# Optimization experiments

Measured on AMD Instinct MI355X. Metric: run time of the kernel, lower is better.

Reference implementation:

```python
import jax, jax.numpy as jnp
import numpy as np

N = 50000          # nodes
E = 800000         # edges (avg degree 16)
NODE_IN, NODE_OUT = 64, 96
EDGE_IN, EDGE_OUT = 32, 32
CONV = [192, 192]  # hidden_conv_sizes
LIN = [192]        # hidden_linear_sizes
NUM_CLASSES = 2


def _linear_init(k, fan_in, fan_out):
    s = 1.0 / np.sqrt(fan_in)
    kw, kb = jax.random.split(k)
    W = jax.random.uniform(kw, (fan_in, fan_out), jnp.float32, -s, s)
    b = jax.random.uniform(kb, (fan_out,), jnp.float32, -s, s)
    return W, b


def setup_inputs() -> dict:
    key = jax.random.key(0)
    ks = jax.random.split(key, 10)
    node_feats = jax.random.normal(ks[0], (N, NODE_IN), jnp.float32)
    edge_feats = jax.random.normal(ks[1], (E, EDGE_IN), jnp.float32)
    src = jax.random.randint(ks[2], (E,), 0, N)
    dst = jax.random.randint(ks[3], (E,), 0, N)
    Wn, bn = _linear_init(ks[4], NODE_IN, NODE_OUT)
    We, be = _linear_init(ks[5], EDGE_IN, EDGE_OUT)
    Wc0, bc0 = _linear_init(ks[6], NODE_OUT + EDGE_OUT, CONV[0])
    Wc1, bc1 = _linear_init(ks[7], CONV[0], CONV[1])
    Wl0, bl0 = _linear_init(ks[8], CONV[1], LIN[0])
    Wo, bo = _linear_init(ks[9], LIN[0], NUM_CLASSES)
    return dict(node_feats=node_feats, edge_feats=edge_feats,
                Wn=Wn, bn=bn, We=We, be=be,
                Wc0=Wc0, bc0=bc0, Wc1=Wc1, bc1=bc1,
                Wl0=Wl0, bl0=bl0, Wo=Wo, bo=bo,
                src=src, dst=dst)


def reference(node_feats, edge_feats, Wn, bn, We, be, Wc0, bc0, Wc1, bc1,
              Wl0, bl0, Wo, bo, src, dst):
    ones = jnp.ones((E,), jnp.float32)
    deg_in = jnp.clip(jax.ops.segment_sum(ones, dst, num_segments=N), 1.0)
    deg_out = jnp.clip(jax.ops.segment_sum(ones, src, num_segments=N), 1.0)
    inv_in = jax.lax.rsqrt(deg_in)    # D_in^{-1/2}
    inv_out = jax.lax.rsqrt(deg_out)  # D_out^{-1/2}

    # EdgeLayer: per-edge linear, mean-aggregated onto destination nodes
    eh = edge_feats @ We + be                                   # [E, EDGE_OUT]
    edge_h = jax.nn.relu(
        jax.ops.segment_sum(eh, dst, num_segments=N) / deg_in[:, None])

    # NodeEmbeddingLayer: per-node linear
    node_h = jax.nn.relu(node_feats @ Wn + bn)                  # [N, NODE_OUT]

    h = jnp.concatenate([edge_h, node_h], axis=1)               # [N, EDGE_OUT+NODE_OUT]

    # dgl GraphConv (norm='both'): D_in^{-1/2} A D_out^{-1/2} h W + b
    # dropout is identity in eval mode
    for W, b in ((Wc0, bc0), (Wc1, bc1)):
        msg = (h * inv_out[:, None])[src]                       # [E, d] gather
        agg = jax.ops.segment_sum(msg, dst, num_segments=N) * inv_in[:, None]
        h = jax.nn.relu(agg @ W + b)

    h = jax.nn.relu(h @ Wl0 + bl0)
    return h @ Wo + bo                                          # [N, NUM_CLASSES]
```

## Files before the change

### kernel.cpp

```cpp
#include <hip/hip_runtime.h>

#define NN 50000
#define NE 800000
#define CAP 64

#define NPB 128
#define NBKT 391
#define NBKT_PAD 512
#define BCAP 3072
#define CHUNK 4096

typedef unsigned short u16;
typedef unsigned long long u64;
typedef __attribute__((ext_vector_type(8))) short bf8_t;
typedef __attribute__((ext_vector_type(4))) float f4_t;

__device__ __forceinline__ u16 f2b(float f) {
    unsigned u = __float_as_uint(f);
    unsigned r = u + 0x7FFF + ((u >> 16) & 1);
    return (u16)(r >> 16);
}

__global__ __launch_bounds__(256) void partition_k(
    const int* __restrict__ src, const int* __restrict__ dst,
    int* __restrict__ deg_out, int* __restrict__ bktc,
    u64* __restrict__ part, int E) {
    __shared__ unsigned cnt[NBKT_PAD];
    __shared__ unsigned base[NBKT_PAD];
    __shared__ unsigned cur[NBKT_PAD];
    __shared__ unsigned gbase[NBKT_PAD];
    __shared__ unsigned wtot[4];
    __shared__ u64 staged[CHUNK];

    const int tid = threadIdx.x;
    const int lane = tid & 63;
    const int wid = tid >> 6;
    const int e0 = blockIdx.x * CHUNK;
    const int n = min(CHUNK, E - e0);

    for (int i = tid; i < NBKT_PAD; i += 256) cnt[i] = 0;
    __syncthreads();

    for (int i = tid; i < n; i += 256) {
        int d = dst[e0 + i];
        atomicAdd(&cnt[d >> 7], 1u);
    }
    __syncthreads();

    {
        unsigned a = cnt[2 * tid];
        unsigned b = cnt[2 * tid + 1];
        unsigned ps = a + b;
        unsigned inc = ps;
#pragma unroll
        for (int d = 1; d < 64; d <<= 1) {
            unsigned v = __shfl_up(inc, d);
            if (lane >= d) inc += v;
        }
        if (lane == 63) wtot[wid] = inc;
        __syncthreads();
        unsigned wb = 0;
#pragma unroll
        for (int k = 0; k < 4; ++k) wb += (k < wid) ? wtot[k] : 0;
        unsigned eb = wb + inc - ps;
        base[2 * tid] = eb;
        base[2 * tid + 1] = eb + a;
        cur[2 * tid] = eb;
        cur[2 * tid + 1] = eb + a;
    }
    __syncthreads();

    for (int i = tid; i < n; i += 256) {
        int e = e0 + i;
        int d = dst[e];
        int s = src[e];
        atomicAdd(deg_out + s, 1);
        unsigned p = atomicAdd(&cur[d >> 7], 1u);
        staged[p] = ((u64)(unsigned)e << 32) | (((unsigned)d << 16) | (unsigned)s);
    }
    __syncthreads();

    for (int b = tid; b < NBKT; b += 256) {
        unsigned c = cur[b] - base[b];
        if (c) gbase[b] = (unsigned)atomicAdd(&bktc[b], (int)c);
    }
    __syncthreads();

    for (int i = tid; i < n; i += 256) {
        u64 v = staged[i];
        int b = (int)((v >> 16) & 0xffffu) >> 7;
        unsigned idx = gbase[b] + ((unsigned)i - base[b]);
        if (idx < BCAP) part[(size_t)b * BCAP + idx] = v;
    }
}

__global__ __launch_bounds__(256) void fill_k(
    const u64* __restrict__ part, const int* __restrict__ bktc,
    int2* __restrict__ csr, int* __restrict__ din, int n) {
    __shared__ unsigned cur[NPB];
    const int tid = threadIdx.x;
    const int b = blockIdx.x;
    const int node0 = b << 7;
    if (tid < NPB) cur[tid] = 0;
    __syncthreads();

    const int cnt = min(bktc[b], BCAP);
    const u64* p = part + (size_t)b * BCAP;
    for (int i = tid; i < cnt; i += 256) {
        u64 v = p[i];
        int s = (int)(v & 0xffffu);
        int d = (int)((v >> 16) & 0xffffu);
        int e = (int)(v >> 32);
        unsigned q = atomicAdd(&cur[d & (NPB - 1)], 1u);
        if (q < CAP) csr[((size_t)d << 6) + q] = make_int2(s, e);
    }
    __syncthreads();
    int node = node0 + tid;
    if (tid < NPB && node < n) din[node] = (int)cur[tid];
}

__global__ void make_inv_k(const int* __restrict__ deg_in, const int* __restrict__ deg_out,
                           float* __restrict__ inv_in, float* __restrict__ inv_out,
                           float* __restrict__ inv_mean, float* __restrict__ bcoef, int n) {
    int i = blockIdx.x * 256 + threadIdx.x;
    if (i < n) {
        int d_in = deg_in[i];
        float di = fmaxf((float)d_in, 1.0f);
        float dq = fmaxf((float)deg_out[i], 1.0f);
        inv_in[i]   = 1.0f / sqrtf(di);
        inv_out[i]  = 1.0f / sqrtf(dq);
        inv_mean[i] = 1.0f / di;
        bcoef[i]    = (d_in > 0) ? 1.0f : 0.0f;
    }
}

__global__ __launch_bounds__(256) void gather_e2_k(
    const float* __restrict__ ef, const int2* __restrict__ csr,
    const int* __restrict__ deg, float* __restrict__ efa) {
    const int lane = threadIdx.x & 63;
    const int node = __builtin_amdgcn_readfirstlane(blockIdx.x * 4 + (threadIdx.x >> 6));
    const int beg = node << 6;
    const int cnt = deg[node];
    const int off = lane & 31;
    const int half = lane >> 5;
    float acc = 0.0f;

    const int np = cnt >> 1;
    const int nb = np >> 3, rem = np & 7;
    int idx[8];
    if (nb > 0) {
#pragma unroll
        for (int j = 0; j < 8; ++j) idx[j] = csr[beg + 2 * j + half].y;
    }
    for (int b = 0; b < nb; ++b) {
        float lv[8];
#pragma unroll
        for (int j = 0; j < 8; ++j) lv[j] = ef[(size_t)idx[j] * 32 + off];
        int nidx[8];
        const int nbase = beg + 2 * (b + 1) * 8;
        if (b + 1 < nb) {
#pragma unroll
            for (int j = 0; j < 8; ++j) nidx[j] = csr[nbase + 2 * j + half].y;
        }
#pragma unroll
        for (int j = 0; j < 8; ++j) acc += lv[j];
        if (b + 1 < nb) {
#pragma unroll
            for (int j = 0; j < 8; ++j) idx[j] = nidx[j];
        }
    }
    const int tbase = beg + 2 * nb * 8;
    for (int t = 0; t < rem; ++t) acc += ef[(size_t)csr[tbase + 2 * t + half].y * 32 + off];
    if ((cnt & 1) && half == 0) acc += ef[(size_t)csr[beg + cnt - 1].y * 32 + off];

    acc += __shfl_down(acc, 32);
    if (lane < 32) efa[(size_t)node * 32 + off] = acc;
}

template <int D, int LPT>
__global__ __launch_bounds__(256) void gather_b2_k(
    const u16* __restrict__ h, const int2* __restrict__ csr,
    const int* __restrict__ deg, const float* __restrict__ inv_in,
    u16* __restrict__ agg) {
    constexpr int ACT = D / LPT;
    constexpr int NW = LPT / 2;
    const int lane = threadIdx.x & 63;
    const int node = __builtin_amdgcn_readfirstlane(blockIdx.x * 4 + (threadIdx.x >> 6));
    const int beg = node << 6;
    const int cnt = deg[node];
    const int off = (lane < ACT ? lane : ACT - 1) * LPT;

    float acc[LPT];
#pragma unroll
    for (int j = 0; j < LPT; ++j) acc[j] = 0.0f;

    const int nb = cnt >> 4;
    int idx[16];
    if (nb > 0) {
#pragma unroll
        for (int j = 0; j < 16; ++j) idx[j] = csr[beg + j].x;
    }
    for (int b = 0; b < nb; ++b) {
        unsigned lv[16][NW];
#pragma unroll
        for (int j = 0; j < 16; ++j) {
            const unsigned* p = (const unsigned*)(h + (size_t)idx[j] * D + off);
            if constexpr (NW == 2) {
                uint2 t = *(const uint2*)p;
                lv[j][0] = t.x; lv[j][1] = t.y;
            } else {
                lv[j][0] = *p;
            }
        }
        int nidx[16];
        const int nbase = beg + (b + 1) * 16;
        if (b + 1 < nb) {
#pragma unroll
            for (int j = 0; j < 16; ++j) nidx[j] = csr[nbase + j].x;
        }
#pragma unroll
        for (int j = 0; j < 16; ++j)
#pragma unroll
            for (int q = 0; q < NW; ++q) {
                unsigned u = lv[j][q];
                acc[2 * q]     += __uint_as_float(u << 16);
                acc[2 * q + 1] += __uint_as_float(u & 0xffff0000u);
            }
        if (b + 1 < nb) {
#pragma unroll
            for (int j = 0; j < 16; ++j) idx[j] = nidx[j];
        }
    }

    int tb = beg + (nb << 4);
    int rem = cnt & 15;
    if (rem >= 8) {
        int ti[8];
#pragma unroll
        for (int j = 0; j < 8; ++j) ti[j] = csr[tb + j].x;
        unsigned lv[8][NW];
#pragma unroll
        for (int j = 0; j < 8; ++j) {
            const unsigned* p = (const unsigned*)(h + (size_t)ti[j] * D + off);
            if constexpr (NW == 2) {
                uint2 t = *(const uint2*)p;
                lv[j][0] = t.x; lv[j][1] = t.y;
            } else {
                lv[j][0] = *p;
            }
        }
#pragma unroll
        for (int j = 0; j < 8; ++j)
#pragma unroll
            for (int q = 0; q < NW; ++q) {
                unsigned u = lv[j][q];
                acc[2 * q]     += __uint_as_float(u << 16);
                acc[2 * q + 1] += __uint_as_float(u & 0xffff0000u);
            }
        tb += 8;
        rem -= 8;
    }
    for (int t = 0; t < rem; ++t) {
        const unsigned* p = (const unsigned*)(h + (size_t)csr[tb + t].x * D + off);
#pragma unroll
        for (int q = 0; q < NW; ++q) {
            unsigned u = p[q];
            acc[2 * q]     += __uint_as_float(u << 16);
            acc[2 * q + 1] += __uint_as_float(u & 0xffff0000u);
        }
    }

    if (lane < ACT) {
        float sc = inv_in[node];
        unsigned o[NW];
#pragma unroll
        for (int q = 0; q < NW; ++q)
            o[q] = (unsigned)f2b(acc[2 * q] * sc) | ((unsigned)f2b(acc[2 * q + 1] * sc) << 16);
        unsigned* dp = (unsigned*)(agg + (size_t)node * D + off);
        if constexpr (NW == 2) {
            uint2 t; t.x = o[0]; t.y = o[1];
            *(uint2*)dp = t;
        } else {
            *dp = o[0];
        }
    }
}

template <int D_IN, int D_OUT, bool SCALE, bool BROW>
__global__ __launch_bounds__(256) void gemm_tile_k(
    const float* __restrict__ in, int in_stride,
    const float* __restrict__ W, const float* __restrict__ bias,
    const float* __restrict__ scale, const float* __restrict__ brow,
    const float* __restrict__ posts,
    u16* __restrict__ out, int out_stride, int n) {
    constexpr int TMW = 8;
    constexpr int ROWS = TMW * 4;
    constexpr int NOUT = (D_OUT + 63) / 64;
    __shared__ float s_in[ROWS * D_IN];

    const int tid = threadIdx.x;
    const int lane = tid & 63;
    const int wave = tid >> 6;
    const int row0 = blockIdx.x * ROWS;

    constexpr int NV = ROWS * D_IN / 4;
    for (int i = tid; i < NV; i += 256) {
        int m = i / (D_IN / 4);
        int kv = i % (D_IN / 4);
        int row = min(row0 + m, n - 1);
        float4 v = *(const float4*)(in + (size_t)row * in_stride + kv * 4);
        if (SCALE) {
            float s = scale[row];
            v.x *= s; v.y *= s; v.z *= s; v.w *= s;
        }
        *(float4*)(s_in + m * D_IN + kv * 4) = v;
    }
    __syncthreads();

    int f[NOUT], ff[NOUT];
    bool fok[NOUT];
    float bv[NOUT];
#pragma unroll
    for (int o = 0; o < NOUT; ++o) {
        f[o] = lane + 64 * o;
        fok[o] = (f[o] < D_OUT);
        ff[o] = fok[o] ? f[o] : 0;
        bv[o] = bias[ff[o]];
    }

    const float* s_my = s_in + wave * TMW * D_IN;

    float acc[NOUT][TMW];
#pragma unroll
    for (int o = 0; o < NOUT; ++o)
#pragma unroll
        for (int m = 0; m < TMW; ++m) acc[o][m] = 0.0f;

    for (int k = 0; k < D_IN; k += 4) {
        float w[4][NOUT];
#pragma unroll
        for (int j = 0; j < 4; ++j)
#pragma unroll
            for (int o = 0; o < NOUT; ++o) w[j][o] = W[(k + j) * D_OUT + ff[o]];
#pragma unroll
        for (int m = 0; m < TMW; ++m) {
            float4 a = *(const float4*)(s_my + m * D_IN + k);
#pragma unroll
            for (int o = 0; o < NOUT; ++o) {
                acc[o][m] = fmaf(a.x, w[0][o], acc[o][m]);
                acc[o][m] = fmaf(a.y, w[1][o], acc[o][m]);
                acc[o][m] = fmaf(a.z, w[2][o], acc[o][m]);
                acc[o][m] = fmaf(a.w, w[3][o], acc[o][m]);
            }
        }
    }

#pragma unroll
    for (int m = 0; m < TMW; ++m) {
        int row = row0 + wave * TMW + m;
        if (row < n) {
            float bc = BROW ? brow[row] : 1.0f;
            float pm = posts[row];
#pragma unroll
            for (int o = 0; o < NOUT; ++o) {
                if (!fok[o]) continue;
                float v = fmaxf(acc[o][m] + bv[o] * bc, 0.0f) * pm;
                out[(size_t)row * out_stride + f[o]] = f2b(v);
            }
        }
    }
}

template <int K>
__global__ void pack_w_k(const float* __restrict__ W, u16* __restrict__ Wp) {
    constexpr int KS = K / 32;
    int idx = blockIdx.x * 256 + threadIdx.x;
    if (idx >= 12 * KS * 64) return;
    int l = idx & 63;
    int s = (idx >> 6) % KS;
    int t = (idx >> 6) / KS;
    int col = t * 16 + (l & 15);
    int krow = s * 32 + ((l >> 4) * 8);
    u16 tmp[8] __attribute__((aligned(16)));
#pragma unroll
    for (int j = 0; j < 8; ++j) tmp[j] = f2b(W[(size_t)(krow + j) * 192 + col]);
    *(uint4*)(Wp + (size_t)idx * 8) = *(const uint4*)tmp;
}

template <int K>
__global__ __launch_bounds__(256) void mfma_gemm_k(
    const u16* __restrict__ A, const u16* __restrict__ Wp,
    const float* __restrict__ bias, const float* __restrict__ posts,
    u16* __restrict__ outB, int n) {
    constexpr int KS = K / 32;
    const int tid = threadIdx.x;
    const int lane = tid & 63;
    const int w = tid >> 6;
    const int row0 = blockIdx.x * 16;
    const int arow = row0 + (lane & 15);
    const int kbase = (lane >> 4) * 8;

    f4_t acc[3];
#pragma unroll
    for (int o = 0; o < 3; ++o) acc[o] = (f4_t){0.f, 0.f, 0.f, 0.f};

    const u16* ap = A + (size_t)arow * K + kbase;
#pragma unroll
    for (int s = 0; s < KS; ++s) {
        bf8_t af = *(const bf8_t*)(ap + s * 32);
#pragma unroll
        for (int o = 0; o < 3; ++o) {
            int t = w * 3 + o;
            bf8_t bf = *(const bf8_t*)(Wp + (size_t)((t * KS + s) * 64 + lane) * 8);
            acc[o] = __builtin_amdgcn_mfma_f32_16x16x32_bf16(af, bf, acc[o], 0, 0, 0);
        }
    }

    const int drow = row0 + (lane >> 4) * 4;
    const int dcol = lane & 15;
    float pm[4];
#pragma unroll
    for (int r = 0; r < 4; ++r) pm[r] = posts[drow + r];
#pragma unroll
    for (int o = 0; o < 3; ++o) {
        int col = (w * 3 + o) * 16 + dcol;
        float bv = bias[col];
#pragma unroll
        for (int r = 0; r < 4; ++r) {
            float v = fmaxf(acc[o][r] + bv, 0.0f) * pm[r];
            outB[(size_t)(drow + r) * 192 + col] = f2b(v);
        }
    }
}

__global__ __launch_bounds__(256) void mfma_fused_k(
    const u16* __restrict__ A,
    const u16* __restrict__ Wp1, const float* __restrict__ b1,
    const u16* __restrict__ Wp2, const float* __restrict__ b2,
    const float* __restrict__ Wo, const float* __restrict__ bo,
    float* __restrict__ out, int n) {
    constexpr int KS = 6;
    constexpr int S = 200;
    __shared__ float sbuf[16 * S];
    __shared__ float s_head[16][17][2];

    const int tid = threadIdx.x;
    const int lane = tid & 63;
    const int w = tid >> 6;
    const int row0 = blockIdx.x * 16;
    const int arow = row0 + (lane & 15);
    const int kbase = (lane >> 4) * 8;
    const int drow = (lane >> 4) * 4;
    const int dcol = lane & 15;

    f4_t acc[3];
#pragma unroll
    for (int o = 0; o < 3; ++o) acc[o] = (f4_t){0.f, 0.f, 0.f, 0.f};

    const u16* ap = A + (size_t)arow * 192 + kbase;
#pragma unroll
    for (int s = 0; s < KS; ++s) {
        bf8_t af = *(const bf8_t*)(ap + s * 32);
#pragma unroll
        for (int o = 0; o < 3; ++o) {
            int t = w * 3 + o;
            bf8_t bf = *(const bf8_t*)(Wp1 + (size_t)((t * KS + s) * 64 + lane) * 8);
            acc[o] = __builtin_amdgcn_mfma_f32_16x16x32_bf16(af, bf, acc[o], 0, 0, 0);
        }
    }

    u16* h2 = (u16*)sbuf;
#pragma unroll
    for (int o = 0; o < 3; ++o) {
        int col = (w * 3 + o) * 16 + dcol;
        float bv = b1[col];
#pragma unroll
        for (int r = 0; r < 4; ++r)
            h2[(drow + r) * S + col] = f2b(fmaxf(acc[o][r] + bv, 0.0f));
    }
    __syncthreads();

#pragma unroll
    for (int o = 0; o < 3; ++o) acc[o] = (f4_t){0.f, 0.f, 0.f, 0.f};
    const u16* hp = h2 + (lane & 15) * S + kbase;
#pragma unroll
    for (int s = 0; s < KS; ++s) {
        bf8_t af = *(const bf8_t*)(hp + s * 32);
#pragma unroll
        for (int o = 0; o < 3; ++o) {
            int t = w * 3 + o;
            bf8_t bf = *(const bf8_t*)(Wp2 + (size_t)((t * KS + s) * 64 + lane) * 8);
            acc[o] = __builtin_amdgcn_mfma_f32_16x16x32_bf16(af, bf, acc[o], 0, 0, 0);
        }
    }
    __syncthreads();

#pragma unroll
    for (int o = 0; o < 3; ++o) {
        int col = (w * 3 + o) * 16 + dcol;
        float bv = b2[col];
#pragma unroll
        for (int r = 0; r < 4; ++r)
            sbuf[(drow + r) * S + col] = fmaxf(acc[o][r] + bv, 0.0f);
    }
    __syncthreads();

    {
        int r = tid >> 4;
        int seg = tid & 15;
        const float* hr = sbuf + r * S + seg * 12;
        const float* wor = Wo + seg * 24;
        float p0 = 0.0f, p1 = 0.0f;
#pragma unroll
        for (int c = 0; c < 12; ++c) {
            float hv = hr[c];
            p0 = fmaf(hv, wor[c * 2 + 0], p0);
            p1 = fmaf(hv, wor[c * 2 + 1], p1);
        }
        s_head[r][seg][0] = p0;
        s_head[r][seg][1] = p1;
    }
    __syncthreads();
    if (tid < 32) {
        int r = tid >> 1, c = tid & 1;
        float sum = bo[c];
#pragma unroll
        for (int g = 0; g < 16; ++g) sum += s_head[r][g][c];
        int row = row0 + r;
        if (row < n) out[(size_t)row * 2 + c] = sum;
    }
}

extern "C" void kernel_launch(void* const* d_in, const int* in_sizes, int n_in,
                              void* d_out, int out_size, void* d_ws, size_t ws_size,
                              hipStream_t stream) {
    const float* node_feats = (const float*)d_in[0];
    const float* edge_feats = (const float*)d_in[1];
    const float* Wn  = (const float*)d_in[2];
    const float* bn  = (const float*)d_in[3];
    const float* We  = (const float*)d_in[4];
    const float* be  = (const float*)d_in[5];
    const float* Wc0 = (const float*)d_in[6];
    const float* bc0 = (const float*)d_in[7];
    const float* Wc1 = (const float*)d_in[8];
    const float* bc1 = (const float*)d_in[9];
    const float* Wl0 = (const float*)d_in[10];
    const float* bl0 = (const float*)d_in[11];
    const float* Wo  = (const float*)d_in[12];
    const float* bo  = (const float*)d_in[13];
    const int* src = (const int*)d_in[14];
    const int* dst = (const int*)d_in[15];
    float* out = (float*)d_out;

    const int N = NN, E = NE;

    int* dout      = (int*)d_ws;
    int* bktc      = dout + N;
    int* din       = bktc + NBKT_PAD;
    int2* csr      = (int2*)(din + N);
    float* inv_in   = (float*)(csr + (size_t)CAP * N);
    float* inv_out  = inv_in + N;
    float* inv_mean = inv_out + N;
    float* bcoef    = inv_mean + N;
    float* efa      = bcoef + N;
    u16* h0   = (u16*)(efa + (size_t)32 * N);
    u16* aggA = h0 + (size_t)128 * N;
    u16* h1   = aggA + (size_t)128 * N;
    u16* aggB = h1 + (size_t)192 * N;
    u16* Wp0  = aggB + (size_t)192 * N;
    u16* Wp1  = Wp0 + 128 * 192;
    u16* Wp2  = Wp1 + 192 * 192;
    u64* part = (u64*)h1;

    hipMemsetAsync(d_ws, 0, (size_t)(N + NBKT_PAD) * sizeof(int), stream);

    const int GB32 = (N + 31) / 32;
    const int GB16 = N / 16;
    const int GW4  = (N + 3) / 4;

    pack_w_k<128><<<dim3(12), dim3(256), 0, stream>>>(Wc0, Wp0);
    pack_w_k<192><<<dim3(18), dim3(256), 0, stream>>>(Wc1, Wp1);
    pack_w_k<192><<<dim3(18), dim3(256), 0, stream>>>(Wl0, Wp2);

    partition_k<<<dim3((E + CHUNK - 1) / CHUNK), dim3(256), 0, stream>>>(
        src, dst, dout, bktc, part, E);
    fill_k<<<dim3(NBKT), dim3(256), 0, stream>>>(part, bktc, csr, din, N);
    make_inv_k<<<dim3((N + 255) / 256), dim3(256), 0, stream>>>(din, dout, inv_in, inv_out,
                                                                inv_mean, bcoef, N);

    gather_e2_k<<<dim3(GW4), dim3(256), 0, stream>>>(edge_feats, csr, din, efa);
    gemm_tile_k<32, 32, true, true><<<dim3(GB32), dim3(256), 0, stream>>>(
        efa, 32, We, be, inv_mean, bcoef, inv_out, h0, 128, N);
    gemm_tile_k<64, 96, false, false><<<dim3(GB32), dim3(256), 0, stream>>>(
        node_feats, 64, Wn, bn, nullptr, nullptr, inv_out, h0 + 32, 128, N);

    gather_b2_k<128, 2><<<dim3(GW4), dim3(256), 0, stream>>>(h0, csr, din, inv_in, aggA);
    mfma_gemm_k<128><<<dim3(GB16), dim3(256), 0, stream>>>(aggA, Wp0, bc0, inv_out, h1, N);

    gather_b2_k<192, 4><<<dim3(GW4), dim3(256), 0, stream>>>(h1, csr, din, inv_in, aggB);
    mfma_fused_k<<<dim3(GB16), dim3(256), 0, stream>>>(aggB, Wp1, bc1, Wp2, bl0, Wo, bo,
                                                       out, N);
}
```

Baseline: 437.2 us.

## Scatter edge features with atomics and shrink CSR entries to source index only

```diff
diff --git a/kernel.cpp b/kernel.cpp
--- a/kernel.cpp
+++ b/kernel.cpp
@@ -11,7 +11,7 @@
 #define CHUNK 4096
 
 typedef unsigned short u16;
-typedef unsigned long long u64;
+typedef unsigned int u32;
 typedef __attribute__((ext_vector_type(8))) short bf8_t;
 typedef __attribute__((ext_vector_type(4))) float f4_t;
 
@@ -21,16 +21,40 @@
     return (u16)(r >> 16);
 }
 
+__global__ __launch_bounds__(256) void edge_agg_k(
+    const float* __restrict__ ef, const int* __restrict__ dst,
+    float* __restrict__ efa, int E) {
+    const int lane = threadIdx.x & 63;
+    const int wv = blockIdx.x * 4 + (threadIdx.x >> 6);
+    const int e0 = wv * 32;
+    if (e0 >= E) return;
+    const int off = lane & 31;
+    const int half = lane >> 5;
+
+    int myd = 0;
+    if (lane < 32) myd = dst[e0 + lane];
+
+    float v[16];
+#pragma unroll
+    for (int j = 0; j < 16; ++j)
+        v[j] = ef[(size_t)(e0 + 2 * j + half) * 32 + off];
+#pragma unroll
+    for (int j = 0; j < 16; ++j) {
+        int d = __shfl(myd, 2 * j + half);
+        atomicAdd(efa + (size_t)d * 32 + off, v[j]);
+    }
+}
+
 __global__ __launch_bounds__(256) void partition_k(
     const int* __restrict__ src, const int* __restrict__ dst,
     int* __restrict__ deg_out, int* __restrict__ bktc,
-    u64* __restrict__ part, int E) {
+    u32* __restrict__ part, int E) {
     __shared__ unsigned cnt[NBKT_PAD];
     __shared__ unsigned base[NBKT_PAD];
     __shared__ unsigned cur[NBKT_PAD];
     __shared__ unsigned gbase[NBKT_PAD];
     __shared__ unsigned wtot[4];
-    __shared__ u64 staged[CHUNK];
+    __shared__ u32 staged[CHUNK];
 
     const int tid = threadIdx.x;
     const int lane = tid & 63;
@@ -76,7 +100,7 @@
         int s = src[e];
         atomicAdd(deg_out + s, 1);
         unsigned p = atomicAdd(&cur[d >> 7], 1u);
-        staged[p] = ((u64)(unsigned)e << 32) | (((unsigned)d << 16) | (unsigned)s);
+        staged[p] = ((u32)d << 16) | (u32)s;
     }
     __syncthreads();
 
@@ -87,16 +111,16 @@
     __syncthreads();
 
     for (int i = tid; i < n; i += 256) {
-        u64 v = staged[i];
-        int b = (int)((v >> 16) & 0xffffu) >> 7;
+        u32 v = staged[i];
+        int b = (int)(v >> 23);
         unsigned idx = gbase[b] + ((unsigned)i - base[b]);
         if (idx < BCAP) part[(size_t)b * BCAP + idx] = v;
     }
 }
 
 __global__ __launch_bounds__(256) void fill_k(
-    const u64* __restrict__ part, const int* __restrict__ bktc,
-    int2* __restrict__ csr, int* __restrict__ din, int n) {
+    const u32* __restrict__ part, const int* __restrict__ bktc,
+    int* __restrict__ csr, int* __restrict__ din, int n) {
     __shared__ unsigned cur[NPB];
     const int tid = threadIdx.x;
     const int b = blockIdx.x;
@@ -105,14 +129,13 @@
     __syncthreads();
 
     const int cnt = min(bktc[b], BCAP);
-    const u64* p = part + (size_t)b * BCAP;
+    const u32* p = part + (size_t)b * BCAP;
     for (int i = tid; i < cnt; i += 256) {
-        u64 v = p[i];
+        u32 v = p[i];
         int s = (int)(v & 0xffffu);
-        int d = (int)((v >> 16) & 0xffffu);
-        int e = (int)(v >> 32);
+        int d = (int)(v >> 16);
         unsigned q = atomicAdd(&cur[d & (NPB - 1)], 1u);
-        if (q < CAP) csr[((size_t)d << 6) + q] = make_int2(s, e);
+        if (q < CAP) csr[((size_t)d << 6) + q] = s;
     }
     __syncthreads();
     int node = node0 + tid;
@@ -134,52 +157,9 @@
     }
 }
 
-__global__ __launch_bounds__(256) void gather_e2_k(
-    const float* __restrict__ ef, const int2* __restrict__ csr,
-    const int* __restrict__ deg, float* __restrict__ efa) {
-    const int lane = threadIdx.x & 63;
-    const int node = __builtin_amdgcn_readfirstlane(blockIdx.x * 4 + (threadIdx.x >> 6));
-    const int beg = node << 6;
-    const int cnt = deg[node];
-    const int off = lane & 31;
-    const int half = lane >> 5;
-    float acc = 0.0f;
-
-    const int np = cnt >> 1;
-    const int nb = np >> 3, rem = np & 7;
-    int idx[8];
-    if (nb > 0) {
-#pragma unroll
-        for (int j = 0; j < 8; ++j) idx[j] = csr[beg + 2 * j + half].y;
-    }
-    for (int b = 0; b < nb; ++b) {
-        float lv[8];
-#pragma unroll
-        for (int j = 0; j < 8; ++j) lv[j] = ef[(size_t)idx[j] * 32 + off];
-        int nidx[8];
-        const int nbase = beg + 2 * (b + 1) * 8;
-        if (b + 1 < nb) {
-#pragma unroll
-            for (int j = 0; j < 8; ++j) nidx[j] = csr[nbase + 2 * j + half].y;
-        }
-#pragma unroll
-        for (int j = 0; j < 8; ++j) acc += lv[j];
-        if (b + 1 < nb) {
-#pragma unroll
-            for (int j = 0; j < 8; ++j) idx[j] = nidx[j];
-        }
-    }
-    const int tbase = beg + 2 * nb * 8;
-    for (int t = 0; t < rem; ++t) acc += ef[(size_t)csr[tbase + 2 * t + half].y * 32 + off];
-    if ((cnt & 1) && half == 0) acc += ef[(size_t)csr[beg + cnt - 1].y * 32 + off];
-
-    acc += __shfl_down(acc, 32);
-    if (lane < 32) efa[(size_t)node * 32 + off] = acc;
-}
-
 template <int D, int LPT>
 __global__ __launch_bounds__(256) void gather_b2_k(
-    const u16* __restrict__ h, const int2* __restrict__ csr,
+    const u16* __restrict__ h, const int* __restrict__ csr,
     const int* __restrict__ deg, const float* __restrict__ inv_in,
     u16* __restrict__ agg) {
     constexpr int ACT = D / LPT;
@@ -198,7 +178,7 @@
     int idx[16];
     if (nb > 0) {
 #pragma unroll
-        for (int j = 0; j < 16; ++j) idx[j] = csr[beg + j].x;
+        for (int j = 0; j < 16; ++j) idx[j] = csr[beg + j];
     }
     for (int b = 0; b < nb; ++b) {
         unsigned lv[16][NW];
@@ -216,7 +196,7 @@
         const int nbase = beg + (b + 1) * 16;
         if (b + 1 < nb) {
 #pragma unroll
-            for (int j = 0; j < 16; ++j) nidx[j] = csr[nbase + j].x;
+            for (int j = 0; j < 16; ++j) nidx[j] = csr[nbase + j];
         }
 #pragma unroll
         for (int j = 0; j < 16; ++j)
@@ -237,7 +217,7 @@
     if (rem >= 8) {
         int ti[8];
 #pragma unroll
-        for (int j = 0; j < 8; ++j) ti[j] = csr[tb + j].x;
+        for (int j = 0; j < 8; ++j) ti[j] = csr[tb + j];
         unsigned lv[8][NW];
 #pragma unroll
         for (int j = 0; j < 8; ++j) {
@@ -261,7 +241,7 @@
         rem -= 8;
     }
     for (int t = 0; t < rem; ++t) {
-        const unsigned* p = (const unsigned*)(h + (size_t)csr[tb + t].x * D + off);
+        const unsigned* p = (const unsigned*)(h + (size_t)csr[tb + t] * D + off);
 #pragma unroll
         for (int q = 0; q < NW; ++q) {
             unsigned u = p[q];
@@ -556,31 +536,34 @@
 
     int* dout      = (int*)d_ws;
     int* bktc      = dout + N;
-    int* din       = bktc + NBKT_PAD;
-    int2* csr      = (int2*)(din + N);
+    float* efa     = (float*)(bktc + NBKT_PAD);
+    int* din       = (int*)(efa + (size_t)32 * N);
+    int* csr       = din + N;
     float* inv_in   = (float*)(csr + (size_t)CAP * N);
     float* inv_out  = inv_in + N;
     float* inv_mean = inv_out + N;
     float* bcoef    = inv_mean + N;
-    float* efa      = bcoef + N;
-    u16* h0   = (u16*)(efa + (size_t)32 * N);
+    u16* h0   = (u16*)(bcoef + N);
     u16* aggA = h0 + (size_t)128 * N;
     u16* h1   = aggA + (size_t)128 * N;
     u16* aggB = h1 + (size_t)192 * N;
     u16* Wp0  = aggB + (size_t)192 * N;
     u16* Wp1  = Wp0 + 128 * 192;
     u16* Wp2  = Wp1 + 192 * 192;
-    u64* part = (u64*)h1;
-
-    hipMemsetAsync(d_ws, 0, (size_t)(N + NBKT_PAD) * sizeof(int), stream);
+    u32* part = (u32*)h1;
+
+    hipMemsetAsync(d_ws, 0, (size_t)(N + NBKT_PAD + (size_t)32 * N) * sizeof(int), stream);
 
     const int GB32 = (N + 31) / 32;
     const int GB16 = N / 16;
     const int GW4  = (N + 3) / 4;
+    const int GEA  = (E / 32 + 3) / 4;
 
     pack_w_k<128><<<dim3(12), dim3(256), 0, stream>>>(Wc0, Wp0);
     pack_w_k<192><<<dim3(18), dim3(256), 0, stream>>>(Wc1, Wp1);
     pack_w_k<192><<<dim3(18), dim3(256), 0, stream>>>(Wl0, Wp2);
+
+    edge_agg_k<<<dim3(GEA), dim3(256), 0, stream>>>(edge_feats, dst, efa, E);
 
     partition_k<<<dim3((E + CHUNK - 1) / CHUNK), dim3(256), 0, stream>>>(
         src, dst, dout, bktc, part, E);
@@ -588,7 +571,6 @@
     make_inv_k<<<dim3((N + 255) / 256), dim3(256), 0, stream>>>(din, dout, inv_in, inv_out,
                                                                 inv_mean, bcoef, N);
 
-    gather_e2_k<<<dim3(GW4), dim3(256), 0, stream>>>(edge_feats, csr, din, efa);
     gemm_tile_k<32, 32, true, true><<<dim3(GB32), dim3(256), 0, stream>>>(
         efa, 32, We, be, inv_mean, bcoef, inv_out, h0, 128, N);
     gemm_tile_k<64, 96, false, false><<<dim3(GB32), dim3(256), 0, stream>>>(
```

Result: slower. 455.9 us (+4.3%).

## Split CSR into separate src/eid arrays and rewrite edge gather with padded fixed-trip loads

Applied to the files above, without the earlier changes.

```diff
diff --git a/kernel.cpp b/kernel.cpp
--- a/kernel.cpp
+++ b/kernel.cpp
@@ -11,6 +11,7 @@
 #define CHUNK 4096
 
 typedef unsigned short u16;
+typedef unsigned int u32;
 typedef unsigned long long u64;
 typedef __attribute__((ext_vector_type(8))) short bf8_t;
 typedef __attribute__((ext_vector_type(4))) float f4_t;
@@ -76,7 +77,7 @@
         int s = src[e];
         atomicAdd(deg_out + s, 1);
         unsigned p = atomicAdd(&cur[d >> 7], 1u);
-        staged[p] = ((u64)(unsigned)e << 32) | (((unsigned)d << 16) | (unsigned)s);
+        staged[p] = ((u64)(unsigned)e << 32) | (((u32)d << 16) | (u32)s);
     }
     __syncthreads();
 
@@ -96,7 +97,8 @@
 
 __global__ __launch_bounds__(256) void fill_k(
     const u64* __restrict__ part, const int* __restrict__ bktc,
-    int2* __restrict__ csr, int* __restrict__ din, int n) {
+    int* __restrict__ csr_src, int* __restrict__ csr_eid,
+    int* __restrict__ din, int n) {
     __shared__ unsigned cur[NPB];
     const int tid = threadIdx.x;
     const int b = blockIdx.x;
@@ -112,11 +114,22 @@
         int d = (int)((v >> 16) & 0xffffu);
         int e = (int)(v >> 32);
         unsigned q = atomicAdd(&cur[d & (NPB - 1)], 1u);
-        if (q < CAP) csr[((size_t)d << 6) + q] = make_int2(s, e);
-    }
-    __syncthreads();
-    int node = node0 + tid;
-    if (tid < NPB && node < n) din[node] = (int)cur[tid];
+        if (q < CAP) {
+            csr_src[((size_t)d << 6) + q] = s;
+            csr_eid[((size_t)d << 6) + q] = e;
+        }
+    }
+    __syncthreads();
+    if (tid < NPB) {
+        int node = node0 + tid;
+        if (node < n) {
+            unsigned cq = min(cur[tid], (unsigned)CAP);
+            din[node] = (int)cq;
+            int end = (cq <= 32u) ? 32 : 64;
+            for (int q = (int)cq; q < end; ++q)
+                csr_eid[((size_t)node << 6) + q] = 0;
+        }
+    }
 }
 
 __global__ void make_inv_k(const int* __restrict__ deg_in, const int* __restrict__ deg_out,
@@ -134,52 +147,52 @@
     }
 }
 
-__global__ __launch_bounds__(256) void gather_e2_k(
-    const float* __restrict__ ef, const int2* __restrict__ csr,
+__global__ __launch_bounds__(256) void gather_e4_k(
+    const float* __restrict__ ef, const int* __restrict__ csr_eid,
     const int* __restrict__ deg, float* __restrict__ efa) {
     const int lane = threadIdx.x & 63;
     const int node = __builtin_amdgcn_readfirstlane(blockIdx.x * 4 + (threadIdx.x >> 6));
     const int beg = node << 6;
     const int cnt = deg[node];
-    const int off = lane & 31;
-    const int half = lane >> 5;
-    float acc = 0.0f;
-
-    const int np = cnt >> 1;
-    const int nb = np >> 3, rem = np & 7;
-    int idx[8];
-    if (nb > 0) {
-#pragma unroll
-        for (int j = 0; j < 8; ++j) idx[j] = csr[beg + 2 * j + half].y;
-    }
-    for (int b = 0; b < nb; ++b) {
-        float lv[8];
-#pragma unroll
-        for (int j = 0; j < 8; ++j) lv[j] = ef[(size_t)idx[j] * 32 + off];
-        int nidx[8];
-        const int nbase = beg + 2 * (b + 1) * 8;
-        if (b + 1 < nb) {
-#pragma unroll
-            for (int j = 0; j < 8; ++j) nidx[j] = csr[nbase + 2 * j + half].y;
-        }
-#pragma unroll
-        for (int j = 0; j < 8; ++j) acc += lv[j];
-        if (b + 1 < nb) {
-#pragma unroll
-            for (int j = 0; j < 8; ++j) idx[j] = nidx[j];
-        }
-    }
-    const int tbase = beg + 2 * nb * 8;
-    for (int t = 0; t < rem; ++t) acc += ef[(size_t)csr[tbase + 2 * t + half].y * 32 + off];
-    if ((cnt & 1) && half == 0) acc += ef[(size_t)csr[beg + cnt - 1].y * 32 + off];
-
-    acc += __shfl_down(acc, 32);
-    if (lane < 32) efa[(size_t)node * 32 + off] = acc;
+    const int g = lane >> 4;
+    const int c = (lane & 15) * 2;
+
+    float ax = 0.0f, ay = 0.0f;
+    {
+        int eidv[8];
+#pragma unroll
+        for (int j = 0; j < 8; ++j) eidv[j] = csr_eid[beg + 4 * j + g];
+        float2 v[8];
+#pragma unroll
+        for (int j = 0; j < 8; ++j)
+            v[j] = *(const float2*)(ef + (size_t)eidv[j] * 32 + c);
+#pragma unroll
+        for (int j = 0; j < 8; ++j)
+            if (4 * j + g < cnt) { ax += v[j].x; ay += v[j].y; }
+    }
+    if (cnt > 32) {
+        int eidv[8];
+#pragma unroll
+        for (int j = 0; j < 8; ++j) eidv[j] = csr_eid[beg + 32 + 4 * j + g];
+        float2 v[8];
+#pragma unroll
+        for (int j = 0; j < 8; ++j)
+            v[j] = *(const float2*)(ef + (size_t)eidv[j] * 32 + c);
+#pragma unroll
+        for (int j = 0; j < 8; ++j)
+            if (32 + 4 * j + g < cnt) { ax += v[j].x; ay += v[j].y; }
+    }
+    ax += __shfl_down(ax, 16); ay += __shfl_down(ay, 16);
+    ax += __shfl_down(ax, 32); ay += __shfl_down(ay, 32);
+    if (lane < 16) {
+        float2 o; o.x = ax; o.y = ay;
+        *(float2*)(efa + (size_t)node * 32 + c) = o;
+    }
 }
 
 template <int D, int LPT>
 __global__ __launch_bounds__(256) void gather_b2_k(
-    const u16* __restrict__ h, const int2* __restrict__ csr,
+    const u16* __restrict__ h, const int* __restrict__ csr,
     const int* __restrict__ deg, const float* __restrict__ inv_in,
     u16* __restrict__ agg) {
     constexpr int ACT = D / LPT;
@@ -198,7 +211,7 @@
     int idx[16];
     if (nb > 0) {
 #pragma unroll
-        for (int j = 0; j < 16; ++j) idx[j] = csr[beg + j].x;
+        for (int j = 0; j < 16; ++j) idx[j] = csr[beg + j];
     }
     for (int b = 0; b < nb; ++b) {
         unsigned lv[16][NW];
@@ -216,7 +229,7 @@
         const int nbase = beg + (b + 1) * 16;
         if (b + 1 < nb) {
 #pragma unroll
-            for (int j = 0; j < 16; ++j) nidx[j] = csr[nbase + j].x;
+            for (int j = 0; j < 16; ++j) nidx[j] = csr[nbase + j];
         }
 #pragma unroll
         for (int j = 0; j < 16; ++j)
@@ -237,7 +250,7 @@
     if (rem >= 8) {
         int ti[8];
 #pragma unroll
-        for (int j = 0; j < 8; ++j) ti[j] = csr[tb + j].x;
+        for (int j = 0; j < 8; ++j) ti[j] = csr[tb + j];
         unsigned lv[8][NW];
 #pragma unroll
         for (int j = 0; j < 8; ++j) {
@@ -261,7 +274,7 @@
         rem -= 8;
     }
     for (int t = 0; t < rem; ++t) {
-        const unsigned* p = (const unsigned*)(h + (size_t)csr[tb + t].x * D + off);
+        const unsigned* p = (const unsigned*)(h + (size_t)csr[tb + t] * D + off);
 #pragma unroll
         for (int q = 0; q < NW; ++q) {
             unsigned u = p[q];
@@ -557,8 +570,9 @@
     int* dout      = (int*)d_ws;
     int* bktc      = dout + N;
     int* din       = bktc + NBKT_PAD;
-    int2* csr      = (int2*)(din + N);
-    float* inv_in   = (float*)(csr + (size_t)CAP * N);
+    int* csr_src   = din + N;
+    int* csr_eid   = csr_src + (size_t)CAP * N;
+    float* inv_in   = (float*)(csr_eid + (size_t)CAP * N);
     float* inv_out  = inv_in + N;
     float* inv_mean = inv_out + N;
     float* bcoef    = inv_mean + N;
@@ -584,20 +598,21 @@
 
     partition_k<<<dim3((E + CHUNK - 1) / CHUNK), dim3(256), 0, stream>>>(
         src, dst, dout, bktc, part, E);
-    fill_k<<<dim3(NBKT), dim3(256), 0, stream>>>(part, bktc, csr, din, N);
+    fill_k<<<dim3(NBKT), dim3(256), 0, stream>>>(part, bktc, csr_src, csr_eid, din, N);
     make_inv_k<<<dim3((N + 255) / 256), dim3(256), 0, stream>>>(din, dout, inv_in, inv_out,
                                                                 inv_mean, bcoef, N);
 
-    gather_e2_k<<<dim3(GW4), dim3(256), 0, stream>>>(edge_feats, csr, din, efa);
+    gather_e4_k<<<dim3(GW4), dim3(256), 0, stream>>>(edge_feats, csr_eid, din, efa);
+
     gemm_tile_k<32, 32, true, true><<<dim3(GB32), dim3(256), 0, stream>>>(
         efa, 32, We, be, inv_mean, bcoef, inv_out, h0, 128, N);
     gemm_tile_k<64, 96, false, false><<<dim3(GB32), dim3(256), 0, stream>>>(
         node_feats, 64, Wn, bn, nullptr, nullptr, inv_out, h0 + 32, 128, N);
 
-    gather_b2_k<128, 2><<<dim3(GW4), dim3(256), 0, stream>>>(h0, csr, din, inv_in, aggA);
+    gather_b2_k<128, 2><<<dim3(GW4), dim3(256), 0, stream>>>(h0, csr_src, din, inv_in, aggA);
     mfma_gemm_k<128><<<dim3(GB16), dim3(256), 0, stream>>>(aggA, Wp0, bc0, inv_out, h1, N);
 
-    gather_b2_k<192, 4><<<dim3(GW4), dim3(256), 0, stream>>>(h1, csr, din, inv_in, aggB);
+    gather_b2_k<192, 4><<<dim3(GW4), dim3(256), 0, stream>>>(h1, csr_src, din, inv_in, aggB);
     mfma_fused_k<<<dim3(GB16), dim3(256), 0, stream>>>(aggB, Wp1, bc1, Wp2, bl0, Wo, bo,
                                                        out, N);
 }
```

Result: no change. 429.6 us (-1.8%).
